# Kernel tuning notes

Hardware: AMD Instinct MI355X
Metric: run time of the kernel (lower is better)

Reference implementation:

```python
import jax, jax.numpy as jnp
import numpy as np

B, D, N, H, K = 8192, 1024, 4096, 8, 4
T, DECAY, STEPS = 100.0, 0.001, 3


def setup_inputs() -> dict:
    key = jax.random.key(0)
    ks = jax.random.split(key, 16)
    rn = lambda k, sh, s=0.02: jax.random.normal(k, sh, jnp.float32) * s
    return {
        'query': jax.random.normal(ks[0], (B, D), jnp.float32),
        'wm': jax.random.normal(ks[1], (B, D), jnp.float32),
        'keys': jax.random.normal(ks[2], (N, D), jnp.float32) * 0.1,
        'values': jax.random.normal(ks[3], (N, D), jnp.float32) * 0.1,
        'last_access': jax.random.uniform(ks[4], (N,), jnp.float32) * T,
        'importance': jnp.ones((N,), jnp.float32),
        'consolid': jnp.ones((N,), jnp.float32),
        'emo_tags': jax.random.uniform(ks[5], (N, 8), jnp.float32),
        'active': jnp.ones((N,), jnp.float32),
        'in_proj_w': rn(ks[6], (3 * D, D)), 'in_proj_b': jnp.zeros((3 * D,), jnp.float32),
        'out_w': rn(ks[7], (D, D)), 'out_b': jnp.zeros((D,), jnp.float32),
        'msg_w1': rn(ks[8], (D, 2 * D)), 'msg_b1': jnp.zeros((D,), jnp.float32),
        'msg_ln_g': jnp.ones((D,), jnp.float32), 'msg_ln_b': jnp.zeros((D,), jnp.float32),
        'msg_w2': rn(ks[9], (D, D)), 'msg_b2': jnp.zeros((D,), jnp.float32),
        'gru_wih': rn(ks[10], (3 * D, D)), 'gru_whh': rn(ks[11], (3 * D, D)),
        'gru_bih': jnp.zeros((3 * D,), jnp.float32), 'gru_bhh': jnp.zeros((3 * D,), jnp.float32),
        'rsn_w1': rn(ks[12], (D, D)), 'rsn_b1': jnp.zeros((D,), jnp.float32),
        'rsn_ln_g': jnp.ones((D,), jnp.float32), 'rsn_ln_b': jnp.zeros((D,), jnp.float32),
        'rsn_w2': rn(ks[13], (D, D)), 'rsn_b2': jnp.zeros((D,), jnp.float32),
        'top_k': K,
    }


def _ln(x, g, b):
    m = x.mean(-1, keepdims=True)
    v = ((x - m) ** 2).mean(-1, keepdims=True)
    return (x - m) / jnp.sqrt(v + 1e-5) * g + b


def reference(query, wm, keys, values, last_access, importance, consolid, emo_tags, active,
              in_proj_w, in_proj_b, out_w, out_b,
              msg_w1, msg_b1, msg_ln_g, msg_ln_b, msg_w2, msg_b2,
              gru_wih, gru_whh, gru_bih, gru_bhh,
              rsn_w1, rsn_b1, rsn_ln_g, rsn_ln_b, rsn_w2, rsn_b2, top_k):
    sg = jax.lax.stop_gradient
    # --- schema retrieve: cosine sim + forgetting-decay + boosts + topk softmax gather ---
    qn = query / jnp.maximum(jnp.linalg.norm(query, axis=-1, keepdims=True), 1e-8)
    kn = keys / jnp.maximum(jnp.linalg.norm(keys, axis=-1, keepdims=True), 1e-8)
    sims = qn @ kn.T  # [B, N]
    forget = sg(jnp.exp(-DECAY * (T - last_access)))
    boost = sg(emo_tags.sum(-1) * 0.1 + importance * 0.2 + jnp.log1p(consolid) * 0.1)
    scores = (sims * forget + boost) * sg(active)
    top_s, top_i = jax.lax.top_k(scores, top_k)  # [B, K]
    w = jax.nn.softmax(top_s, axis=-1)
    schema = jnp.einsum('bk,bkd->bd', w, values[top_i])  # [B, D]

    # --- GraphReasoner: 3 steps of 2-token MHA + msg_net + GRUCell ---
    dh = D // H
    scale = 1.0 / np.sqrt(dh).astype(np.float32)

    def mha(x):  # x [B, 2, D]
        qkv = x @ in_proj_w.T + in_proj_b
        q, k, v = jnp.split(qkv, 3, axis=-1)
        q = q.reshape(-1, 2, H, dh); k = k.reshape(-1, 2, H, dh); v = v.reshape(-1, 2, H, dh)
        a = jax.nn.softmax(jnp.einsum('bqhd,bkhd->bhqk', q, k) * scale, axis=-1)
        o = jnp.einsum('bhqk,bkhd->bqhd', a, v).reshape(-1, 2, D)
        return o @ out_w.T + out_b

    def gru(x, h):
        gi = x @ gru_wih.T + gru_bih
        gh = h @ gru_whh.T + gru_bhh
        ir, iz, inn = jnp.split(gi, 3, axis=-1)
        hr, hz, hn = jnp.split(gh, 3, axis=-1)
        r = jax.nn.sigmoid(ir + hr)
        z = jax.nn.sigmoid(iz + hz)
        n = jnp.tanh(inn + r * hn)
        return (1.0 - z) * n + z * h

    state = wm
    for _ in range(STEPS):
        ctx = jnp.stack([state, schema], axis=1)  # [B, 2, D]
        att = mha(ctx)
        combined = jnp.concatenate([att[:, 0], att[:, 1]], axis=-1)  # [B, 2D]
        msg = jax.nn.relu(_ln(combined @ msg_w1.T + msg_b1, msg_ln_g, msg_ln_b)) @ msg_w2.T + msg_b2
        state = gru(msg, state)
    out = jax.nn.relu(_ln(state @ rsn_w1.T + rsn_b1, rsn_ln_g, rsn_ln_b)) @ rsn_w2.T + rsn_b2
    return out
```

## Files before the change

### kernel.cpp

```cpp
#include <hip/hip_runtime.h>
#include <cstdint>
#include <cstddef>

typedef __attribute__((ext_vector_type(8))) short short8;
typedef __attribute__((ext_vector_type(4))) float f32x4;
typedef __attribute__((ext_vector_type(4))) unsigned short us4;

#define DEVINL static __device__ __forceinline__
#define AS1 __attribute__((address_space(1)))
#define AS3 __attribute__((address_space(3)))

DEVINL float bf2f(unsigned short u){
  union { unsigned uu; float f; } v; v.uu = ((unsigned)u) << 16; return v.f;
}
DEVINL unsigned short f2bf(float f){
  unsigned u = __float_as_uint(f);
  u += 0x7fffu + ((u >> 16) & 1u);
  return (unsigned short)(u >> 16);
}

DEVINL bool tk_better(float av, int ai, float bv, int bi){
  return (av > bv) || (av == bv && ai < bi);
}
DEVINL void tk_cmpex(float& va, int& ia, float& vb, int& ib){
  if (!tk_better(va, ia, vb, ib)){
    float tv = va; va = vb; vb = tv;
    int t = ia; ia = ib; ib = t;
  }
}
DEVINL void tk_sort4(float* v, int* id){
  tk_cmpex(v[0], id[0], v[1], id[1]);
  tk_cmpex(v[2], id[2], v[3], id[3]);
  tk_cmpex(v[0], id[0], v[2], id[2]);
  tk_cmpex(v[1], id[1], v[3], id[3]);
  tk_cmpex(v[1], id[1], v[2], id[2]);
}
DEVINL void tk_bmerge(float* v, int* id, const float* pv, const int* pi){
  #pragma unroll
  for (int i = 0; i < 4; ++i){
    bool ta = tk_better(v[i], id[i], pv[3 - i], pi[3 - i]);
    v[i]  = ta ? v[i]  : pv[3 - i];
    id[i] = ta ? id[i] : pi[3 - i];
  }
  tk_cmpex(v[0], id[0], v[2], id[2]);
  tk_cmpex(v[1], id[1], v[3], id[3]);
  tk_cmpex(v[0], id[0], v[1], id[1]);
  tk_cmpex(v[2], id[2], v[3], id[3]);
}

__global__ void k_diag(float* out, float v){ out[0] = v; }

__global__ __launch_bounds__(256) void k_cast_bf16(const float* __restrict__ x,
                                                   unsigned short* __restrict__ y, int n4){
  int stride = gridDim.x * blockDim.x;
  for (int i = blockIdx.x * blockDim.x + threadIdx.x; i < n4; i += stride){
    float4 v = ((const float4*)x)[i];
    us4 o; o[0] = f2bf(v.x); o[1] = f2bf(v.y); o[2] = f2bf(v.z); o[3] = f2bf(v.w);
    ((us4*)y)[i] = o;
  }
}

__global__ __launch_bounds__(256) void k_tcast(const float* __restrict__ in,
    unsigned short* __restrict__ outT, int R, int C){
  __shared__ float t[32][33];
  const int bc = blockIdx.x * 32, br = blockIdx.y * 32;
  const int lx = threadIdx.x & 31, ly = threadIdx.x >> 5;
  #pragma unroll
  for (int i = 0; i < 32; i += 8)
    t[ly + i][lx] = in[(size_t)(br + ly + i) * C + bc + lx];
  __syncthreads();
  #pragma unroll
  for (int i = 0; i < 32; i += 8)
    outT[(size_t)(bc + ly + i) * R + br + lx] = f2bf(t[lx][ly + i]);
}

__global__ __launch_bounds__(256) void k_bias_pre(const float* __restrict__ w1,
    const float* __restrict__ outb, const float* __restrict__ b1, float* __restrict__ bc){
  int wave = threadIdx.x >> 6, lane = threadIdx.x & 63;
  int j = blockIdx.x * 4 + wave;
  float s = 0.f;
  for (int m = lane; m < 2048; m += 64)
    s += w1[(size_t)j * 2048 + m] * outb[m & 1023];
  #pragma unroll
  for (int m = 32; m >= 1; m >>= 1) s += __shfl_xor(s, m);
  if (lane == 0) bc[j] = s + b1[j];
}

__global__ __launch_bounds__(256) void k_bias_gi(const float* __restrict__ wih,
    const float* __restrict__ b2, const float* __restrict__ bih, float* __restrict__ bc){
  int wave = threadIdx.x >> 6, lane = threadIdx.x & 63;
  int n = blockIdx.x * 4 + wave;
  float s = 0.f;
  for (int m = lane; m < 1024; m += 64)
    s += wih[(size_t)n * 1024 + m] * b2[m];
  #pragma unroll
  for (int m = 32; m >= 1; m >>= 1) s += __shfl_xor(s, m);
  if (lane == 0) bc[n] = s + bih[n];
}

__global__ __launch_bounds__(256) void k_prep_keys(const float* __restrict__ keys,
    const float* __restrict__ last_access, const float* __restrict__ importance,
    const float* __restrict__ consolid, const float* __restrict__ emo,
    const float* __restrict__ active, float* __restrict__ ascale, float* __restrict__ bbias){
  int wave = threadIdx.x >> 6, lane = threadIdx.x & 63;
  int n = blockIdx.x * 4 + wave;
  const float* kr = keys + (size_t)n * 1024;
  float s = 0.f;
  #pragma unroll
  for (int j = 0; j < 4; ++j){
    float4 v = ((const float4*)kr)[j * 64 + lane];
    s += v.x*v.x + v.y*v.y + v.z*v.z + v.w*v.w;
  }
  #pragma unroll
  for (int m = 32; m >= 1; m >>= 1) s += __shfl_xor(s, m);
  if (lane == 0){
    float norm = fmaxf(sqrtf(s), 1e-8f);
    float forget = expf(-0.001f * (100.0f - last_access[n]));
    float bo = 0.f;
    #pragma unroll
    for (int j = 0; j < 8; ++j) bo += emo[n * 8 + j];
    bo = bo * 0.1f + importance[n] * 0.2f + log1pf(consolid[n]) * 0.1f;
    float a = active[n];
    ascale[n] = forget * a / norm;
    bbias[n]  = bo * a;
  }
}

__global__ __launch_bounds__(256) void k_qnorm(const float* __restrict__ q, float* __restrict__ qinv){
  int wave = threadIdx.x >> 6, lane = threadIdx.x & 63;
  int b = blockIdx.x * 4 + wave;
  const float* qr = q + (size_t)b * 1024;
  float s = 0.f;
  #pragma unroll
  for (int j = 0; j < 4; ++j){
    float4 v = ((const float4*)qr)[j * 64 + lane];
    s += v.x*v.x + v.y*v.y + v.z*v.z + v.w*v.w;
  }
  #pragma unroll
  for (int m = 32; m >= 1; m >>= 1) s += __shfl_xor(s, m);
  if (lane == 0) qinv[b] = 1.0f / fmaxf(sqrtf(s), 1e-8f);
}

__global__ __launch_bounds__(256) void k_split(const float* __restrict__ X,
    const float* __restrict__ rscale, unsigned short* __restrict__ Hi,
    unsigned short* __restrict__ Lo){
  const int row = blockIdx.x;
  const float sc = rscale ? rscale[row] : 1.0f;
  const int d = threadIdx.x * 4;
  float4 v = *(const float4*)(X + (size_t)row * 1024 + d);
  float xs[4] = {v.x * sc, v.y * sc, v.z * sc, v.w * sc};
  us4 h, l;
  #pragma unroll
  for (int j = 0; j < 4; ++j){
    unsigned short hb = f2bf(xs[j]);
    h[j] = hb;
    l[j] = f2bf(xs[j] - bf2f(hb));
  }
  *(us4*)(Hi + (size_t)row * 1024 + d) = h;
  *(us4*)(Lo + (size_t)row * 1024 + d) = l;
}

__global__ __launch_bounds__(256) void k_scores_mfma(
    const unsigned short* __restrict__ Qhi, const unsigned short* __restrict__ Qlo,
    const unsigned short* __restrict__ Khi, const unsigned short* __restrict__ Klo,
    const float* __restrict__ ascale, const float* __restrict__ bbias,
    float* __restrict__ candV, int* __restrict__ candI){
  __shared__ __align__(16) unsigned short AsH[128 * 32];
  __shared__ __align__(16) unsigned short AsL[128 * 32];
  __shared__ __align__(16) unsigned short BsH[128 * 32];
  __shared__ __align__(16) unsigned short BsL[128 * 32];
  const int tid = threadIdx.x;
  const int wave = tid >> 6, lane = tid & 63;
  const int tM = blockIdx.x, tN = blockIdx.y;
  const int wm_ = wave >> 1, wn_ = wave & 1;
  f32x4 acc[4][4] = {};
  const unsigned short* AH = Qhi + (size_t)tM * 128 * 1024;
  const unsigned short* AL = Qlo + (size_t)tM * 128 * 1024;
  const unsigned short* BH = Khi + (size_t)tN * 128 * 1024;
  const unsigned short* BL = Klo + (size_t)tN * 128 * 1024;
  const int lrow = lane & 15, lk = (lane >> 4) * 8;
  for (int k0 = 0; k0 < 1024; k0 += 32){
    __syncthreads();
    #pragma unroll
    for (int j = 0; j < 2; ++j){
      int c = wave * 128 + j * 64 + lane;
      int row = c >> 2, cp = c & 3;
      size_t go = (size_t)row * 1024 + k0 + cp * 8;
      int lo_ = (wave * 2 + j) * 512;
      __builtin_amdgcn_global_load_lds((const AS1 void*)(AH + go), (AS3 void*)(AsH + lo_), 16, 0, 0);
      __builtin_amdgcn_global_load_lds((const AS1 void*)(AL + go), (AS3 void*)(AsL + lo_), 16, 0, 0);
      __builtin_amdgcn_global_load_lds((const AS1 void*)(BH + go), (AS3 void*)(BsH + lo_), 16, 0, 0);
      __builtin_amdgcn_global_load_lds((const AS1 void*)(BL + go), (AS3 void*)(BsL + lo_), 16, 0, 0);
    }
    __syncthreads();
    short8 ah[4], al[4], bh[4], bl[4];
    #pragma unroll
    for (int mi = 0; mi < 4; ++mi){
      int ro = (wm_ * 64 + mi * 16 + lrow) * 32 + lk;
      ah[mi] = *(const short8*)(AsH + ro);
      al[mi] = *(const short8*)(AsL + ro);
    }
    #pragma unroll
    for (int ni = 0; ni < 4; ++ni){
      int ro = (wn_ * 64 + ni * 16 + lrow) * 32 + lk;
      bh[ni] = *(const short8*)(BsH + ro);
      bl[ni] = *(const short8*)(BsL + ro);
    }
    #pragma unroll
    for (int mi = 0; mi < 4; ++mi)
      #pragma unroll
      for (int ni = 0; ni < 4; ++ni){
        acc[mi][ni] = __builtin_amdgcn_mfma_f32_16x16x32_bf16(ah[mi], bh[ni], acc[mi][ni], 0, 0, 0);
        acc[mi][ni] = __builtin_amdgcn_mfma_f32_16x16x32_bf16(ah[mi], bl[ni], acc[mi][ni], 0, 0, 0);
        acc[mi][ni] = __builtin_amdgcn_mfma_f32_16x16x32_bf16(al[mi], bh[ni], acc[mi][ni], 0, 0, 0);
      }
  }
  const int lc = lane & 15;
  float as_[4], bb_[4]; int cid[4];
  #pragma unroll
  for (int ni = 0; ni < 4; ++ni){
    cid[ni] = tN * 128 + wn_ * 64 + ni * 16 + lc;
    as_[ni] = ascale[cid[ni]];
    bb_[ni] = bbias[cid[ni]];
  }
  #pragma unroll
  for (int mi = 0; mi < 4; ++mi){
    #pragma unroll
    for (int r = 0; r < 4; ++r){
      float v[4]; int id[4];
      #pragma unroll
      for (int ni = 0; ni < 4; ++ni){
        v[ni]  = acc[mi][ni][r] * as_[ni] + bb_[ni];
        id[ni] = cid[ni];
      }
      tk_sort4(v, id);
      #pragma unroll
      for (int mask = 1; mask <= 8; mask <<= 1){
        float pv[4]; int pi_[4];
        #pragma unroll
        for (int j = 0; j < 4; ++j){
          pv[j]  = __shfl_xor(v[j], mask);
          pi_[j] = __shfl_xor(id[j], mask);
        }
        tk_bmerge(v, id, pv, pi_);
      }
      if (lc == 0){
        int row = tM * 128 + wm_ * 64 + mi * 16 + (lane >> 4) * 4 + r;
        size_t cb = (size_t)row * 256 + tN * 8 + wn_ * 4;
        #pragma unroll
        for (int j = 0; j < 4; ++j){ candV[cb + j] = v[j]; candI[cb + j] = id[j]; }
      }
    }
  }
}

__global__ __launch_bounds__(256) void k_topk_merge(const float* __restrict__ candV,
    const int* __restrict__ candI, const float* __restrict__ V,
    unsigned short* __restrict__ schema_bf){
  const int row = blockIdx.x, tid = threadIdx.x;
  const int wave = tid >> 6, lane = tid & 63;
  float v[4]; int id[4];
  v[0] = candV[(size_t)row * 256 + tid];
  id[0] = candI[(size_t)row * 256 + tid];
  #pragma unroll
  for (int j = 1; j < 4; ++j){ v[j] = -3.4e38f; id[j] = 0x7fffffff; }
  #pragma unroll
  for (int mask = 1; mask <= 32; mask <<= 1){
    float pv[4]; int pi_[4];
    #pragma unroll
    for (int j = 0; j < 4; ++j){
      pv[j]  = __shfl_xor(v[j], mask);
      pi_[j] = __shfl_xor(id[j], mask);
    }
    tk_bmerge(v, id, pv, pi_);
  }
  __shared__ float wv[4][4]; __shared__ int wi[4][4];
  if (lane == 0){
    #pragma unroll
    for (int j = 0; j < 4; ++j){ wv[wave][j] = v[j]; wi[wave][j] = id[j]; }
  }
  __syncthreads();
  __shared__ float w_sh[4]; __shared__ int i_sh[4];
  if (tid == 0){
    float fv[4]; int fi[4];
    #pragma unroll
    for (int j = 0; j < 4; ++j){ fv[j] = wv[0][j]; fi[j] = wi[0][j]; }
    #pragma unroll
    for (int w = 1; w < 4; ++w){
      float pv[4]; int pi_[4];
      #pragma unroll
      for (int j = 0; j < 4; ++j){ pv[j] = wv[w][j]; pi_[j] = wi[w][j]; }
      tk_bmerge(fv, fi, pv, pi_);
    }
    float m = fv[0];
    float e0 = expf(fv[0] - m), e1 = expf(fv[1] - m), e2 = expf(fv[2] - m), e3 = expf(fv[3] - m);
    float inv = 1.f / (e0 + e1 + e2 + e3);
    w_sh[0] = e0 * inv; w_sh[1] = e1 * inv; w_sh[2] = e2 * inv; w_sh[3] = e3 * inv;
    i_sh[0] = fi[0]; i_sh[1] = fi[1]; i_sh[2] = fi[2]; i_sh[3] = fi[3];
  }
  __syncthreads();
  float w0 = w_sh[0], w1 = w_sh[1], w2 = w_sh[2], w3 = w_sh[3];
  const float* v0 = V + (size_t)i_sh[0] * 1024;
  const float* v1 = V + (size_t)i_sh[1] * 1024;
  const float* v2 = V + (size_t)i_sh[2] * 1024;
  const float* v3 = V + (size_t)i_sh[3] * 1024;
  int d = tid * 4;
  float4 a = *(const float4*)(v0 + d);
  float4 b4 = *(const float4*)(v1 + d);
  float4 c = *(const float4*)(v2 + d);
  float4 e = *(const float4*)(v3 + d);
  us4 o;
  o[0] = f2bf(w0*a.x + w1*b4.x + w2*c.x + w3*e.x);
  o[1] = f2bf(w0*a.y + w1*b4.y + w2*c.y + w3*e.y);
  o[2] = f2bf(w0*a.z + w1*b4.z + w2*c.z + w3*e.z);
  o[3] = f2bf(w0*a.w + w1*b4.w + w2*c.w + w3*e.w);
  *(us4*)(schema_bf + (size_t)row * 1024 + d) = o;
}

__global__ __launch_bounds__(256) void k_initstate(const float* __restrict__ wm,
    float* __restrict__ st, unsigned short* __restrict__ stbf){
  size_t i = ((size_t)blockIdx.x * 256 + threadIdx.x) * 4;
  float4 v = *(const float4*)(wm + i);
  *(float4*)(st + i) = v;
  us4 o; o[0] = f2bf(v.x); o[1] = f2bf(v.y); o[2] = f2bf(v.z); o[3] = f2bf(v.w);
  *(us4*)(stbf + i) = o;
}

template<int OUT_BF16>
__global__ __launch_bounds__(256) void k_gemm(const unsigned short* __restrict__ A,
    const unsigned short* __restrict__ W, const float* __restrict__ bias,
    void* __restrict__ C, int M, int N, int K, int lda, int ldc){
  __shared__ __align__(16) unsigned short As[128 * 32];
  __shared__ __align__(16) unsigned short Ws[128 * 32];
  const int tid = threadIdx.x;
  const int wave = tid >> 6, lane = tid & 63;
  const int tM = blockIdx.x, tN = blockIdx.y;
  const int wm_ = wave >> 1, wn_ = wave & 1;
  f32x4 acc[4][4] = {};
  const unsigned short* Abase = A + (size_t)tM * 128 * lda;
  const unsigned short* Wbase = W + (size_t)tN * 128 * K;
  const int lrow = lane & 15, lk = (lane >> 4) * 8;
  for (int k0 = 0; k0 < K; k0 += 32){
    __syncthreads();
    #pragma unroll
    for (int j = 0; j < 2; ++j){
      int c = wave * 128 + j * 64 + lane;
      int row = c >> 2, cp = c & 3;
      const unsigned short* ga = Abase + (size_t)row * lda + k0 + cp * 8;
      const unsigned short* gw = Wbase + (size_t)row * K + k0 + cp * 8;
      __builtin_amdgcn_global_load_lds((const AS1 void*)ga, (AS3 void*)(As + (wave * 2 + j) * 512), 16, 0, 0);
      __builtin_amdgcn_global_load_lds((const AS1 void*)gw, (AS3 void*)(Ws + (wave * 2 + j) * 512), 16, 0, 0);
    }
    __syncthreads();
    short8 af[4], bfr[4];
    #pragma unroll
    for (int mi = 0; mi < 4; ++mi)
      af[mi] = *(const short8*)(As + (wm_ * 64 + mi * 16 + lrow) * 32 + lk);
    #pragma unroll
    for (int ni = 0; ni < 4; ++ni)
      bfr[ni] = *(const short8*)(Ws + (wn_ * 64 + ni * 16 + lrow) * 32 + lk);
    #pragma unroll
    for (int mi = 0; mi < 4; ++mi)
      #pragma unroll
      for (int ni = 0; ni < 4; ++ni)
        acc[mi][ni] = __builtin_amdgcn_mfma_f32_16x16x32_bf16(af[mi], bfr[ni], acc[mi][ni], 0, 0, 0);
  }
  const int lc = lane & 15, lr = (lane >> 4) * 4;
  #pragma unroll
  for (int ni = 0; ni < 4; ++ni){
    int col = tN * 128 + wn_ * 64 + ni * 16 + lc;
    float bb = bias ? bias[col] : 0.f;
    #pragma unroll
    for (int mi = 0; mi < 4; ++mi){
      int rowb = tM * 128 + wm_ * 64 + mi * 16 + lr;
      #pragma unroll
      for (int r = 0; r < 4; ++r){
        float vv = acc[mi][ni][r] + bb;
        size_t off = (size_t)(rowb + r) * ldc + col;
        if (OUT_BF16) ((unsigned short*)C)[off] = f2bf(vv);
        else ((float*)C)[off] = vv;
      }
    }
  }
}

template<int OUT_BF16>
__global__ __launch_bounds__(512, 2) void k_gemm8p(const unsigned short* __restrict__ A,
    const unsigned short* __restrict__ W, const float* __restrict__ bias,
    void* __restrict__ C, int M, int N, int K, int lda, int ldc){
  __shared__ __align__(16) unsigned short lds[65536];
  const int tid = threadIdx.x;
  const int wave = tid >> 6, lane = tid & 63;
  const int wqr = wave >> 2, wqc = wave & 3;
  const int lrow = lane & 15, lkk = lane >> 4;

  const int nwg = gridDim.x * gridDim.y;
  int lin = blockIdx.y * gridDim.x + blockIdx.x;
  int cpx = nwg >> 3;
  int swz = (lin & 7) * cpx + (lin >> 3);
  const int nM = M >> 8;
  const int tM = swz % nM, tN = swz / nM;

  const unsigned short* Abase = A + (size_t)tM * 256 * lda;
  const unsigned short* Wbase = W + (size_t)tN * 256 * K;

  f32x4 a00[4][2] = {}, a01[4][2] = {}, a11[4][2] = {}, a10[4][2] = {};
  short8 af[4][2], bf[2][2];
  const int ntiles = K >> 6;

  auto stage = [&](int op, int slot, int half, int tile){
    if (tile >= ntiles) return;
    const unsigned short* G = op ? Wbase : Abase;
    const int rs = op ? K : lda;
    const int k0 = tile * 64, hr = half * 128;
    const int base = op * 32768 + slot * 16384 + half * 8192;
    #pragma unroll
    for (int l = 0; l < 2; ++l){
      int p = l * 512 + tid;
      int row = p >> 3, c = (p & 7) ^ (row & 7);
      int dstc = l * 512 + wave * 64;
      __builtin_amdgcn_global_load_lds(
          (const AS1 void*)(G + (size_t)(hr + row) * rs + k0 + c * 8),
          (AS3 void*)(lds + base + dstc * 8), 16, 0, 0);
    }
  };
  auto ldA = [&](int slot, int half){
    const int base = slot * 16384 + half * 8192;
    #pragma unroll
    for (int mi = 0; mi < 4; ++mi)
      #pragma unroll
      for (int kk = 0; kk < 2; ++kk){
        int row = wqr * 64 + mi * 16 + lrow;
        int c = kk * 4 + lkk;
        af[mi][kk] = *(const short8*)(lds + base + (row * 8 + (c ^ (row & 7))) * 8);
      }
  };
  auto ldB = [&](int slot, int half){
    const int base = 32768 + slot * 16384 + half * 8192;
    #pragma unroll
    for (int ni = 0; ni < 2; ++ni)
      #pragma unroll
      for (int kk = 0; kk < 2; ++kk){
        int row = wqc * 32 + ni * 16 + lrow;
        int c = kk * 4 + lkk;
        bf[ni][kk] = *(const short8*)(lds + base + (row * 8 + (c ^ (row & 7))) * 8);
      }
  };
  auto mfma16 = [&](f32x4 (&acc)[4][2]){
    __builtin_amdgcn_s_setprio(1);
    #pragma unroll
    for (int mi = 0; mi < 4; ++mi)
      #pragma unroll
      for (int ni = 0; ni < 2; ++ni)
        #pragma unroll
        for (int kk = 0; kk < 2; ++kk)
          acc[mi][ni] = __builtin_amdgcn_mfma_f32_16x16x32_bf16(af[mi][kk], bf[ni][kk], acc[mi][ni], 0, 0, 0);
    __builtin_amdgcn_s_setprio(0);
  };
  auto SB = [&](){
    __builtin_amdgcn_sched_barrier(0);
    __builtin_amdgcn_s_barrier();
    __builtin_amdgcn_sched_barrier(0);
  };

  stage(0,0,0, 0); stage(1,0,0, 0); stage(1,0,1, 0); stage(0,0,1, 0);
  stage(0,1,0, 1); stage(1,1,1, 1);
  __builtin_amdgcn_sched_barrier(0);
  asm volatile("s_waitcnt vmcnt(4)" ::: "memory");
  __builtin_amdgcn_s_barrier();
  __builtin_amdgcn_sched_barrier(0);

  for (int j = 0; j < (ntiles >> 1); ++j){
    const int t0 = 2 * j;
    ldA(0,0); ldB(0,0); stage(0,1,1, t0+1);
    SB(); mfma16(a00); SB();
    ldB(0,1); stage(1,1,0, t0+1);
    SB(); mfma16(a01); SB();
    ldA(0,1); stage(0,0,0, t0+2);
    SB(); mfma16(a11); SB();
    ldB(0,0); stage(1,0,1, t0+2);
    SB(); mfma16(a10);
    __builtin_amdgcn_sched_barrier(0);
    if (t0 + 2 < ntiles) asm volatile("s_waitcnt vmcnt(4)" ::: "memory");
    else                 asm volatile("s_waitcnt vmcnt(0)" ::: "memory");
    __builtin_amdgcn_s_barrier();
    __builtin_amdgcn_sched_barrier(0);
    ldA(1,0); ldB(1,0); stage(0,0,1, t0+2);
    SB(); mfma16(a00); SB();
    ldB(1,1); stage(1,0,0, t0+2);
    SB(); mfma16(a01); SB();
    ldA(1,1); stage(0,1,0, t0+3);
    SB(); mfma16(a11); SB();
    ldB(1,0); stage(1,1,1, t0+3);
    SB(); mfma16(a10);
    __builtin_amdgcn_sched_barrier(0);
    asm volatile("s_waitcnt vmcnt(4)" ::: "memory");
    __builtin_amdgcn_s_barrier();
    __builtin_amdgcn_sched_barrier(0);
  }

  const int lc = lane & 15, lr = (lane >> 4) * 4;
  auto wout = [&](f32x4 (&acc)[4][2], int MH, int NH){
    #pragma unroll
    for (int ni = 0; ni < 2; ++ni){
      int col = tN * 256 + NH * 128 + wqc * 32 + ni * 16 + lc;
      float bb = bias ? bias[col] : 0.f;
      #pragma unroll
      for (int mi = 0; mi < 4; ++mi){
        int rowb = tM * 256 + MH * 128 + wqr * 64 + mi * 16 + lr;
        #pragma unroll
        for (int r = 0; r < 4; ++r){
          float vv = acc[mi][ni][r] + bb;
          size_t off = (size_t)(rowb + r) * ldc + col;
          if (OUT_BF16) ((unsigned short*)C)[off] = f2bf(vv);
          else ((float*)C)[off] = vv;
        }
      }
    }
  };
  wout(a00, 0, 0); wout(a01, 0, 1); wout(a11, 1, 1); wout(a10, 1, 0);
}

__global__ __launch_bounds__(256) void k_attn(unsigned short* qgh,
    const unsigned short* __restrict__ qkvM){
  const int b = blockIdx.x, tid = threadIdx.x;
  const int l = tid & 31;
  const int e = (tid >> 5) * 128 + l * 4;
  unsigned short* ps = qgh + (size_t)b * 6144;
  const unsigned short* pm = qkvM + (size_t)b * 3072;
  float q0[4], kk0[4], v0[4], q1[4], kk1[4], v1[4];
  us4 t;
  t = *(const us4*)(ps + e);        for (int j = 0; j < 4; ++j) q0[j]  = bf2f(t[j]);
  t = *(const us4*)(ps + 1024 + e); for (int j = 0; j < 4; ++j) kk0[j] = bf2f(t[j]);
  t = *(const us4*)(ps + 2048 + e); for (int j = 0; j < 4; ++j) v0[j]  = bf2f(t[j]);
  t = *(const us4*)(pm + e);        for (int j = 0; j < 4; ++j) q1[j]  = bf2f(t[j]);
  t = *(const us4*)(pm + 1024 + e); for (int j = 0; j < 4; ++j) kk1[j] = bf2f(t[j]);
  t = *(const us4*)(pm + 2048 + e); for (int j = 0; j < 4; ++j) v1[j]  = bf2f(t[j]);
  float s00 = 0.f, s01 = 0.f, s10 = 0.f, s11 = 0.f;
  #pragma unroll
  for (int j = 0; j < 4; ++j){
    s00 += q0[j] * kk0[j]; s01 += q0[j] * kk1[j];
    s10 += q1[j] * kk0[j]; s11 += q1[j] * kk1[j];
  }
  #pragma unroll
  for (int m = 16; m >= 1; m >>= 1){
    s00 += __shfl_xor(s00, m); s01 += __shfl_xor(s01, m);
    s10 += __shfl_xor(s10, m); s11 += __shfl_xor(s11, m);
  }
  const float sc = 0.08838834764831845f;
  s00 *= sc; s01 *= sc; s10 *= sc; s11 *= sc;
  float m0 = fmaxf(s00, s01), m1 = fmaxf(s10, s11);
  float e00 = expf(s00 - m0), e01 = expf(s01 - m0);
  float e10 = expf(s10 - m1), e11 = expf(s11 - m1);
  float i0 = 1.f / (e00 + e01), i1 = 1.f / (e10 + e11);
  float w00 = e00 * i0, w01 = e01 * i0, w10 = e10 * i1, w11 = e11 * i1;
  us4 o0, o1;
  #pragma unroll
  for (int j = 0; j < 4; ++j){
    o0[j] = f2bf(w00 * v0[j] + w01 * v1[j]);
    o1[j] = f2bf(w10 * v0[j] + w11 * v1[j]);
  }
  *(us4*)(ps + e)        = o0;
  *(us4*)(ps + 1024 + e) = o1;
}

template<int IN_BF16>
__global__ __launch_bounds__(256) void k_ln_relu(const void* X,
    const float* __restrict__ g, const float* __restrict__ bta, unsigned short* Y){
  const int row = blockIdx.x, tid = threadIdx.x;
  const int d = tid * 4;
  float e0, e1, e2, e3;
  if (IN_BF16){
    us4 t = *(const us4*)((const unsigned short*)X + (size_t)row * 1024 + d);
    e0 = bf2f(t[0]); e1 = bf2f(t[1]); e2 = bf2f(t[2]); e3 = bf2f(t[3]);
  } else {
    float4 v = *(const float4*)((const float*)X + (size_t)row * 1024 + d);
    e0 = v.x; e1 = v.y; e2 = v.z; e3 = v.w;
  }
  float s1 = e0 + e1 + e2 + e3;
  float s2 = e0*e0 + e1*e1 + e2*e2 + e3*e3;
  #pragma unroll
  for (int m = 32; m >= 1; m >>= 1){ s1 += __shfl_xor(s1, m); s2 += __shfl_xor(s2, m); }
  __shared__ float a1[4], a2[4];
  int wave = tid >> 6, lane = tid & 63;
  if (lane == 0){ a1[wave] = s1; a2[wave] = s2; }
  __syncthreads();
  s1 = a1[0] + a1[1] + a1[2] + a1[3];
  s2 = a2[0] + a2[1] + a2[2] + a2[3];
  float mean = s1 * (1.f / 1024.f);
  float var  = s2 * (1.f / 1024.f) - mean * mean;
  float rstd = rsqrtf(var + 1e-5f);
  float4 gg = *(const float4*)(g + d);
  float4 bb = *(const float4*)(bta + d);
  us4 o;
  o[0] = f2bf(fmaxf((e0 - mean) * rstd * gg.x + bb.x, 0.f));
  o[1] = f2bf(fmaxf((e1 - mean) * rstd * gg.y + bb.y, 0.f));
  o[2] = f2bf(fmaxf((e2 - mean) * rstd * gg.z + bb.z, 0.f));
  o[3] = f2bf(fmaxf((e3 - mean) * rstd * gg.w + bb.w, 0.f));
  *(us4*)(Y + (size_t)row * 1024 + d) = o;
}

__global__ __launch_bounds__(256) void k_gru(const unsigned short* __restrict__ qgh,
    const float* __restrict__ h, float* __restrict__ hn, unsigned short* __restrict__ hnbf){
  const int b = blockIdx.x;
  const int d = threadIdx.x * 4;
  const unsigned short* pi = qgh + (size_t)b * 6144;
  const unsigned short* ph = pi + 3072;
  us4 t;
  float ir[4], iz[4], in_[4], hr[4], hz[4], hnn[4];
  t = *(const us4*)(pi + d);        for (int j = 0; j < 4; ++j) ir[j]  = bf2f(t[j]);
  t = *(const us4*)(pi + 1024 + d); for (int j = 0; j < 4; ++j) iz[j]  = bf2f(t[j]);
  t = *(const us4*)(pi + 2048 + d); for (int j = 0; j < 4; ++j) in_[j] = bf2f(t[j]);
  t = *(const us4*)(ph + d);        for (int j = 0; j < 4; ++j) hr[j]  = bf2f(t[j]);
  t = *(const us4*)(ph + 1024 + d); for (int j = 0; j < 4; ++j) hz[j]  = bf2f(t[j]);
  t = *(const us4*)(ph + 2048 + d); for (int j = 0; j < 4; ++j) hnn[j] = bf2f(t[j]);
  float4 hv = *(const float4*)(h + (size_t)b * 1024 + d);
  float hvv[4] = {hv.x, hv.y, hv.z, hv.w};
  float ov[4]; us4 ob;
  #pragma unroll
  for (int j = 0; j < 4; ++j){
    float r = 1.f / (1.f + expf(-(ir[j] + hr[j])));
    float z = 1.f / (1.f + expf(-(iz[j] + hz[j])));
    float n = tanhf(in_[j] + r * hnn[j]);
    float o = (1.f - z) * n + z * hvv[j];
    ov[j] = o; ob[j] = f2bf(o);
  }
  float4 of; of.x = ov[0]; of.y = ov[1]; of.z = ov[2]; of.w = ov[3];
  *(float4*)(hn + (size_t)b * 1024 + d) = of;
  *(us4*)(hnbf + (size_t)b * 1024 + d) = ob;
}

extern "C" void kernel_launch(void* const* d_in, const int* in_sizes, int n_in,
                              void* d_out, int out_size, void* d_ws, size_t ws_size,
                              hipStream_t stream) {
  (void)in_sizes; (void)n_in; (void)out_size;
  const float* query       = (const float*)d_in[0];
  const float* wm          = (const float*)d_in[1];
  const float* keys        = (const float*)d_in[2];
  const float* values      = (const float*)d_in[3];
  const float* last_access = (const float*)d_in[4];
  const float* importance  = (const float*)d_in[5];
  const float* consolid    = (const float*)d_in[6];
  const float* emo         = (const float*)d_in[7];
  const float* active      = (const float*)d_in[8];
  const float* in_proj_w   = (const float*)d_in[9];
  const float* in_proj_b   = (const float*)d_in[10];
  const float* out_w       = (const float*)d_in[11];
  const float* out_b       = (const float*)d_in[12];
  const float* msg_w1      = (const float*)d_in[13];
  const float* msg_b1      = (const float*)d_in[14];
  const float* msg_ln_g    = (const float*)d_in[15];
  const float* msg_ln_b    = (const float*)d_in[16];
  const float* msg_w2      = (const float*)d_in[17];
  const float* msg_b2      = (const float*)d_in[18];
  const float* gru_wih     = (const float*)d_in[19];
  const float* gru_whh     = (const float*)d_in[20];
  const float* gru_bih     = (const float*)d_in[21];
  const float* gru_bhh     = (const float*)d_in[22];
  const float* rsn_w1      = (const float*)d_in[23];
  const float* rsn_b1      = (const float*)d_in[24];
  const float* rsn_ln_g    = (const float*)d_in[25];
  const float* rsn_ln_b    = (const float*)d_in[26];
  const float* rsn_w2      = (const float*)d_in[27];
  const float* rsn_b2      = (const float*)d_in[28];
  float* out = (float*)d_out;

  size_t off = 0;
  char* base = (char*)d_ws;
  auto carve = [&](size_t bytes) -> char* {
    char* p = base + off;
    off += (bytes + 255) & ~(size_t)255;
    return p;
  };
  float* ascale = (float*)carve(4096*4);
  float* bbias  = (float*)carve(4096*4);
  float* qinv   = (float*)carve(8192*4);
  float* bc_pre = (float*)carve(1024*4);
  float* bc_gi  = (float*)carve(3072*4);
  float* bc_ih  = (float*)carve(6144*4);
  unsigned short* wb_ihh  = (unsigned short*)carve((size_t)6144*1024*2);
  unsigned short* wb_rw1  = (unsigned short*)carve((size_t)1024*1024*2);
  unsigned short* wb_rw2  = (unsigned short*)carve((size_t)1024*1024*2);
  unsigned short* wb_Wab  = (unsigned short*)carve((size_t)1024*2048*2);
  unsigned short* wb_Wc   = (unsigned short*)carve((size_t)3072*1024*2);
  unsigned short* schema_bf = (unsigned short*)carve((size_t)8192*1024*2);
  float*          state_f   = (float*)carve((size_t)8192*1024*4);
  unsigned short* state_bf  = (unsigned short*)carve((size_t)8192*1024*2);
  unsigned short* qkvM      = (unsigned short*)carve((size_t)8192*3072*2);
  unsigned short* qgh       = (unsigned short*)carve((size_t)8192*6144*2);

  if (off > ws_size){
    k_diag<<<1, 1, 0, stream>>>(out, (float)(ws_size >> 20));
    return;
  }

  unsigned short* tmp_w1bf  = qgh;
  unsigned short* tmp_outwT = qgh + (size_t)1024*2048;
  unsigned short* tmp_w2T   = tmp_outwT + (size_t)1024*1024;
  unsigned short* tmp_wihbf = tmp_w2T + (size_t)1024*1024;

  unsigned short* Qhi = qkvM;
  unsigned short* Qlo = Qhi + (size_t)8192*1024;
  unsigned short* Khi = Qlo + (size_t)8192*1024;
  unsigned short* Klo = Khi + (size_t)4096*1024;
  float* candV = (float*)(qgh + (size_t)8192*3072);
  int*   candI = (int*)((char*)candV + (size_t)8192*256*4);

  unsigned short* preln_h1 = schema_bf;

  auto cast = [&](const float* src, unsigned short* dst, int n){
    k_cast_bf16<<<1024, 256, 0, stream>>>(src, dst, n / 4);
  };
  cast(in_proj_w, wb_ihh,                     3072*1024);
  cast(gru_whh,   wb_ihh + (size_t)3072*1024, 3072*1024);
  cast(rsn_w1,    wb_rw1,    1024*1024);
  cast(rsn_w2,    wb_rw2,    1024*1024);
  cast(msg_w1,    tmp_w1bf,  1024*2048);
  cast(gru_wih,   tmp_wihbf, 3072*1024);
  hipMemcpyAsync(bc_ih,        in_proj_b, 3072*4, hipMemcpyDeviceToDevice, stream);
  hipMemcpyAsync(bc_ih + 3072, gru_bhh,   3072*4, hipMemcpyDeviceToDevice, stream);
  k_tcast<<<dim3(32, 32), 256, 0, stream>>>(out_w,  tmp_outwT, 1024, 1024);
  k_tcast<<<dim3(32, 32), 256, 0, stream>>>(msg_w2, tmp_w2T,   1024, 1024);
  k_bias_pre<<<256, 256, 0, stream>>>(msg_w1, out_b, msg_b1, bc_pre);
  k_bias_gi<<<768, 256, 0, stream>>>(gru_wih, msg_b2, gru_bih, bc_gi);
  k_gemm<1><<<dim3(8, 8), 256, 0, stream>>>(tmp_w1bf,        tmp_outwT, nullptr, wb_Wab,        1024, 1024, 1024, 2048, 2048);
  k_gemm<1><<<dim3(8, 8), 256, 0, stream>>>(tmp_w1bf + 1024, tmp_outwT, nullptr, wb_Wab + 1024, 1024, 1024, 1024, 2048, 2048);
  k_gemm<1><<<dim3(24, 8), 256, 0, stream>>>(tmp_wihbf, tmp_w2T, nullptr, wb_Wc, 3072, 1024, 1024, 1024, 1024);

  k_qnorm<<<2048, 256, 0, stream>>>(query, qinv);
  k_prep_keys<<<1024, 256, 0, stream>>>(keys, last_access, importance, consolid, emo, active, ascale, bbias);
  k_split<<<8192, 256, 0, stream>>>(query, qinv, Qhi, Qlo);
  k_split<<<4096, 256, 0, stream>>>(keys, nullptr, Khi, Klo);
  k_scores_mfma<<<dim3(64, 32), 256, 0, stream>>>(Qhi, Qlo, Khi, Klo, ascale, bbias, candV, candI);
  k_topk_merge<<<8192, 256, 0, stream>>>(candV, candI, values, schema_bf);

  k_initstate<<<8192, 256, 0, stream>>>(wm, state_f, state_bf);
  k_gemm8p<1><<<dim3(32, 12), 512, 0, stream>>>(schema_bf, wb_ihh, bc_ih, qkvM, 8192, 3072, 1024, 1024, 3072);
  for (int s = 0; s < 3; ++s){
    k_gemm8p<1><<<dim3(32, 24), 512, 0, stream>>>(state_bf, wb_ihh, bc_ih, qgh, 8192, 6144, 1024, 1024, 6144);
    k_attn<<<8192, 256, 0, stream>>>(qgh, qkvM);
    k_gemm<1><<<dim3(64, 8), 256, 0, stream>>>(qgh, wb_Wab, bc_pre, preln_h1, 8192, 1024, 2048, 6144, 1024);
    k_ln_relu<1><<<8192, 256, 0, stream>>>(preln_h1, msg_ln_g, msg_ln_b, preln_h1);
    k_gemm8p<1><<<dim3(32, 12), 512, 0, stream>>>(preln_h1, wb_Wc, bc_gi, qgh, 8192, 3072, 1024, 1024, 6144);
    k_gru<<<8192, 256, 0, stream>>>(qgh, state_f, state_f, state_bf);
  }
  float* hpre = (float*)qgh;
  unsigned short* hh1 = qgh + (size_t)8192*3072;
  k_gemm<0><<<dim3(64, 8), 256, 0, stream>>>(state_bf, wb_rw1, rsn_b1, hpre, 8192, 1024, 1024, 1024, 1024);
  k_ln_relu<0><<<8192, 256, 0, stream>>>(hpre, rsn_ln_g, rsn_ln_b, hh1);
  k_gemm<0><<<dim3(64, 8), 256, 0, stream>>>(hh1, wb_rw2, rsn_b2, out, 8192, 1024, 1024, 1024, 1024);
}
```

Before: 1.502 ms.

## Rewrite retrieval scores GEMM as 256x256 pipelined kernel with concatenated split-bf16 K

The split-bf16 query and key operands are now laid out as single 3072-wide rows ([hi|lo|hi] against [hi|hi|lo]), so the three-term compensated product becomes one long-K GEMM. The scores kernel moves from a 128x128 tile with 256 threads and a sync-heavy loop to the 8-wave 256x256 ping-pong kernel. That kernel uses a swizzled LDS layout, double buffering, setprio and explicit waitcnt scheduling. The aim is higher MFMA utilisation and less global traffic per output. The cost is more scratch memory, duplicated hi writes, and a fixed grid of 512 workgroups.

```diff
diff --git a/kernel.cpp b/kernel.cpp
--- a/kernel.cpp
+++ b/kernel.cpp
@@ -141,9 +141,9 @@
   if (lane == 0) qinv[b] = 1.0f / fmaxf(sqrtf(s), 1e-8f);
 }
 
-__global__ __launch_bounds__(256) void k_split(const float* __restrict__ X,
-    const float* __restrict__ rscale, unsigned short* __restrict__ Hi,
-    unsigned short* __restrict__ Lo){
+__global__ __launch_bounds__(256) void k_split3(const float* __restrict__ X,
+    const float* __restrict__ rscale, unsigned short* __restrict__ D,
+    int offH1, int offH2, int offL){
   const int row = blockIdx.x;
   const float sc = rscale ? rscale[row] : 1.0f;
   const int d = threadIdx.x * 4;
@@ -156,102 +156,169 @@
     h[j] = hb;
     l[j] = f2bf(xs[j] - bf2f(hb));
   }
-  *(us4*)(Hi + (size_t)row * 1024 + d) = h;
-  *(us4*)(Lo + (size_t)row * 1024 + d) = l;
-}
-
-__global__ __launch_bounds__(256) void k_scores_mfma(
-    const unsigned short* __restrict__ Qhi, const unsigned short* __restrict__ Qlo,
-    const unsigned short* __restrict__ Khi, const unsigned short* __restrict__ Klo,
-    const float* __restrict__ ascale, const float* __restrict__ bbias,
-    float* __restrict__ candV, int* __restrict__ candI){
-  __shared__ __align__(16) unsigned short AsH[128 * 32];
-  __shared__ __align__(16) unsigned short AsL[128 * 32];
-  __shared__ __align__(16) unsigned short BsH[128 * 32];
-  __shared__ __align__(16) unsigned short BsL[128 * 32];
+  unsigned short* base = D + (size_t)row * 3072;
+  *(us4*)(base + offH1 + d) = h;
+  *(us4*)(base + offH2 + d) = h;
+  *(us4*)(base + offL  + d) = l;
+}
+
+__global__ __launch_bounds__(512, 2) void k_scores8p(const unsigned short* __restrict__ QX,
+    const unsigned short* __restrict__ KX, const float* __restrict__ ascale,
+    const float* __restrict__ bbias, float* __restrict__ candV, int* __restrict__ candI){
+  __shared__ __align__(16) unsigned short lds[65536];
   const int tid = threadIdx.x;
   const int wave = tid >> 6, lane = tid & 63;
-  const int tM = blockIdx.x, tN = blockIdx.y;
-  const int wm_ = wave >> 1, wn_ = wave & 1;
-  f32x4 acc[4][4] = {};
-  const unsigned short* AH = Qhi + (size_t)tM * 128 * 1024;
-  const unsigned short* AL = Qlo + (size_t)tM * 128 * 1024;
-  const unsigned short* BH = Khi + (size_t)tN * 128 * 1024;
-  const unsigned short* BL = Klo + (size_t)tN * 128 * 1024;
-  const int lrow = lane & 15, lk = (lane >> 4) * 8;
-  for (int k0 = 0; k0 < 1024; k0 += 32){
-    __syncthreads();
-    #pragma unroll
-    for (int j = 0; j < 2; ++j){
-      int c = wave * 128 + j * 64 + lane;
-      int row = c >> 2, cp = c & 3;
-      size_t go = (size_t)row * 1024 + k0 + cp * 8;
-      int lo_ = (wave * 2 + j) * 512;
-      __builtin_amdgcn_global_load_lds((const AS1 void*)(AH + go), (AS3 void*)(AsH + lo_), 16, 0, 0);
-      __builtin_amdgcn_global_load_lds((const AS1 void*)(AL + go), (AS3 void*)(AsL + lo_), 16, 0, 0);
-      __builtin_amdgcn_global_load_lds((const AS1 void*)(BH + go), (AS3 void*)(BsH + lo_), 16, 0, 0);
-      __builtin_amdgcn_global_load_lds((const AS1 void*)(BL + go), (AS3 void*)(BsL + lo_), 16, 0, 0);
+  const int wqr = wave >> 2, wqc = wave & 3;
+  const int lrow = lane & 15, lkk = lane >> 4;
+  const int K = 3072;
+
+  const int nwg = gridDim.x * gridDim.y;
+  int lin = blockIdx.y * gridDim.x + blockIdx.x;
+  int cpx = nwg >> 3;
+  int swz = (lin & 7) * cpx + (lin >> 3);
+  const int nM = 32;
+  const int tM = swz % nM, tN = swz / nM;
+
+  const unsigned short* Abase = QX + (size_t)tM * 256 * K;
+  const unsigned short* Wbase = KX + (size_t)tN * 256 * K;
+
+  f32x4 a00[4][2] = {}, a01[4][2] = {}, a11[4][2] = {}, a10[4][2] = {};
+  short8 af[4][2], bf[2][2];
+  const int ntiles = K >> 6;
+
+  auto stage = [&](int op, int slot, int half, int tile){
+    if (tile >= ntiles) return;
+    const unsigned short* G = op ? Wbase : Abase;
+    const int k0 = tile * 64, hr = half * 128;
+    const int base = op * 32768 + slot * 16384 + half * 8192;
+    #pragma unroll
+    for (int l = 0; l < 2; ++l){
+      int p = l * 512 + tid;
+      int row = p >> 3, c = (p & 7) ^ (row & 7);
+      int dstc = l * 512 + wave * 64;
+      __builtin_amdgcn_global_load_lds(
+          (const AS1 void*)(G + (size_t)(hr + row) * K + k0 + c * 8),
+          (AS3 void*)(lds + base + dstc * 8), 16, 0, 0);
     }
-    __syncthreads();
-    short8 ah[4], al[4], bh[4], bl[4];
+  };
+  auto ldA = [&](int slot, int half){
+    const int base = slot * 16384 + half * 8192;
+    #pragma unroll
+    for (int mi = 0; mi < 4; ++mi)
+      #pragma unroll
+      for (int kk = 0; kk < 2; ++kk){
+        int row = wqr * 64 + mi * 16 + lrow;
+        int c = kk * 4 + lkk;
+        af[mi][kk] = *(const short8*)(lds + base + (row * 8 + (c ^ (row & 7))) * 8);
+      }
+  };
+  auto ldB = [&](int slot, int half){
+    const int base = 32768 + slot * 16384 + half * 8192;
+    #pragma unroll
+    for (int ni = 0; ni < 2; ++ni)
+      #pragma unroll
+      for (int kk = 0; kk < 2; ++kk){
+        int row = wqc * 32 + ni * 16 + lrow;
+        int c = kk * 4 + lkk;
+        bf[ni][kk] = *(const short8*)(lds + base + (row * 8 + (c ^ (row & 7))) * 8);
+      }
+  };
+  auto mfma16 = [&](f32x4 (&acc)[4][2]){
+    __builtin_amdgcn_s_setprio(1);
+    #pragma unroll
+    for (int mi = 0; mi < 4; ++mi)
+      #pragma unroll
+      for (int ni = 0; ni < 2; ++ni)
+        #pragma unroll
+        for (int kk = 0; kk < 2; ++kk)
+          acc[mi][ni] = __builtin_amdgcn_mfma_f32_16x16x32_bf16(af[mi][kk], bf[ni][kk], acc[mi][ni], 0, 0, 0);
+    __builtin_amdgcn_s_setprio(0);
+  };
+  auto SB = [&](){
+    __builtin_amdgcn_sched_barrier(0);
+    __builtin_amdgcn_s_barrier();
+    __builtin_amdgcn_sched_barrier(0);
+  };
+
+  stage(0,0,0, 0); stage(1,0,0, 0); stage(1,0,1, 0); stage(0,0,1, 0);
+  stage(0,1,0, 1); stage(1,1,1, 1);
+  __builtin_amdgcn_sched_barrier(0);
+  asm volatile("s_waitcnt vmcnt(4)" ::: "memory");
+  __builtin_amdgcn_s_barrier();
+  __builtin_amdgcn_sched_barrier(0);
+
+  for (int j = 0; j < (ntiles >> 1); ++j){
+    const int t0 = 2 * j;
+    ldA(0,0); ldB(0,0); stage(0,1,1, t0+1);
+    SB(); mfma16(a00); SB();
+    ldB(0,1); stage(1,1,0, t0+1);
+    SB(); mfma16(a01); SB();
+    ldA(0,1); stage(0,0,0, t0+2);
+    SB(); mfma16(a11); SB();
+    ldB(0,0); stage(1,0,1, t0+2);
+    SB(); mfma16(a10);
+    __builtin_amdgcn_sched_barrier(0);
+    if (t0 + 2 < ntiles) asm volatile("s_waitcnt vmcnt(4)" ::: "memory");
+    else                 asm volatile("s_waitcnt vmcnt(0)" ::: "memory");
+    __builtin_amdgcn_s_barrier();
+    __builtin_amdgcn_sched_barrier(0);
+    ldA(1,0); ldB(1,0); stage(0,0,1, t0+2);
+    SB(); mfma16(a00); SB();
+    ldB(1,1); stage(1,0,0, t0+2);
+    SB(); mfma16(a01); SB();
+    ldA(1,1); stage(0,1,0, t0+3);
+    SB(); mfma16(a11); SB();
+    ldB(1,0); stage(1,1,1, t0+3);
+    SB(); mfma16(a10);
+    __builtin_amdgcn_sched_barrier(0);
+    asm volatile("s_waitcnt vmcnt(4)" ::: "memory");
+    __builtin_amdgcn_s_barrier();
+    __builtin_amdgcn_sched_barrier(0);
+  }
+
+  const int lc = lane & 15, lgrp = lane >> 4;
+  float as_[2][2], bb_[2][2]; int cid[2][2];
+  #pragma unroll
+  for (int NH = 0; NH < 2; ++NH)
+    #pragma unroll
+    for (int ni = 0; ni < 2; ++ni){
+      int col = tN * 256 + NH * 128 + wqc * 32 + ni * 16 + lc;
+      cid[NH][ni] = col;
+      as_[NH][ni] = ascale[col];
+      bb_[NH][ni] = bbias[col];
+    }
+  auto epi = [&](f32x4 (&n0)[4][2], f32x4 (&n1)[4][2], int MH){
     #pragma unroll
     for (int mi = 0; mi < 4; ++mi){
-      int ro = (wm_ * 64 + mi * 16 + lrow) * 32 + lk;
-      ah[mi] = *(const short8*)(AsH + ro);
-      al[mi] = *(const short8*)(AsL + ro);
-    }
-    #pragma unroll
-    for (int ni = 0; ni < 4; ++ni){
-      int ro = (wn_ * 64 + ni * 16 + lrow) * 32 + lk;
-      bh[ni] = *(const short8*)(BsH + ro);
-      bl[ni] = *(const short8*)(BsL + ro);
-    }
-    #pragma unroll
-    for (int mi = 0; mi < 4; ++mi)
-      #pragma unroll
-      for (int ni = 0; ni < 4; ++ni){
-        acc[mi][ni] = __builtin_amdgcn_mfma_f32_16x16x32_bf16(ah[mi], bh[ni], acc[mi][ni], 0, 0, 0);
-        acc[mi][ni] = __builtin_amdgcn_mfma_f32_16x16x32_bf16(ah[mi], bl[ni], acc[mi][ni], 0, 0, 0);
-        acc[mi][ni] = __builtin_amdgcn_mfma_f32_16x16x32_bf16(al[mi], bh[ni], acc[mi][ni], 0, 0, 0);
-      }
-  }
-  const int lc = lane & 15;
-  float as_[4], bb_[4]; int cid[4];
-  #pragma unroll
-  for (int ni = 0; ni < 4; ++ni){
-    cid[ni] = tN * 128 + wn_ * 64 + ni * 16 + lc;
-    as_[ni] = ascale[cid[ni]];
-    bb_[ni] = bbias[cid[ni]];
-  }
-  #pragma unroll
-  for (int mi = 0; mi < 4; ++mi){
-    #pragma unroll
-    for (int r = 0; r < 4; ++r){
-      float v[4]; int id[4];
-      #pragma unroll
-      for (int ni = 0; ni < 4; ++ni){
-        v[ni]  = acc[mi][ni][r] * as_[ni] + bb_[ni];
-        id[ni] = cid[ni];
-      }
-      tk_sort4(v, id);
-      #pragma unroll
-      for (int mask = 1; mask <= 8; mask <<= 1){
-        float pv[4]; int pi_[4];
+      #pragma unroll
+      for (int r = 0; r < 4; ++r){
+        float v[4]; int id[4];
+        v[0] = n0[mi][0][r] * as_[0][0] + bb_[0][0]; id[0] = cid[0][0];
+        v[1] = n0[mi][1][r] * as_[0][1] + bb_[0][1]; id[1] = cid[0][1];
+        v[2] = n1[mi][0][r] * as_[1][0] + bb_[1][0]; id[2] = cid[1][0];
+        v[3] = n1[mi][1][r] * as_[1][1] + bb_[1][1]; id[3] = cid[1][1];
+        tk_sort4(v, id);
         #pragma unroll
-        for (int j = 0; j < 4; ++j){
-          pv[j]  = __shfl_xor(v[j], mask);
-          pi_[j] = __shfl_xor(id[j], mask);
+        for (int mask = 1; mask <= 8; mask <<= 1){
+          float pv[4]; int pi_[4];
+          #pragma unroll
+          for (int jj = 0; jj < 4; ++jj){
+            pv[jj]  = __shfl_xor(v[jj], mask);
+            pi_[jj] = __shfl_xor(id[jj], mask);
+          }
+          tk_bmerge(v, id, pv, pi_);
         }
-        tk_bmerge(v, id, pv, pi_);
-      }
-      if (lc == 0){
-        int row = tM * 128 + wm_ * 64 + mi * 16 + (lane >> 4) * 4 + r;
-        size_t cb = (size_t)row * 256 + tN * 8 + wn_ * 4;
-        #pragma unroll
-        for (int j = 0; j < 4; ++j){ candV[cb + j] = v[j]; candI[cb + j] = id[j]; }
+        if (lc == 0){
+          int row = tM * 256 + MH * 128 + wqr * 64 + mi * 16 + lgrp * 4 + r;
+          size_t cb = (size_t)row * 256 + tN * 16 + wqc * 4;
+          #pragma unroll
+          for (int jj = 0; jj < 4; ++jj){ candV[cb + jj] = v[jj]; candI[cb + jj] = id[jj]; }
+        }
       }
     }
-  }
+  };
+  epi(a00, a01, 0);
+  epi(a10, a11, 1);
 }
 
 __global__ __launch_bounds__(256) void k_topk_merge(const float* __restrict__ candV,
@@ -694,15 +761,13 @@
     return;
   }
 
-  unsigned short* tmp_w1bf  = qgh;
-  unsigned short* tmp_outwT = qgh + (size_t)1024*2048;
+  unsigned short* tmp_w1bf  = qgh + (size_t)8192*3072;
+  unsigned short* tmp_outwT = tmp_w1bf + (size_t)1024*2048;
   unsigned short* tmp_w2T   = tmp_outwT + (size_t)1024*1024;
   unsigned short* tmp_wihbf = tmp_w2T + (size_t)1024*1024;
 
-  unsigned short* Qhi = qkvM;
-  unsigned short* Qlo = Qhi + (size_t)8192*1024;
-  unsigned short* Khi = Qlo + (size_t)8192*1024;
-  unsigned short* Klo = Khi + (size_t)4096*1024;
+  unsigned short* QX = qkvM;
+  unsigned short* KX = qgh;
   float* candV = (float*)(qgh + (size_t)8192*3072);
   int*   candI = (int*)((char*)candV + (size_t)8192*256*4);
 
@@ -729,9 +794,9 @@
 
   k_qnorm<<<2048, 256, 0, stream>>>(query, qinv);
   k_prep_keys<<<1024, 256, 0, stream>>>(keys, last_access, importance, consolid, emo, active, ascale, bbias);
-  k_split<<<8192, 256, 0, stream>>>(query, qinv, Qhi, Qlo);
-  k_split<<<4096, 256, 0, stream>>>(keys, nullptr, Khi, Klo);
-  k_scores_mfma<<<dim3(64, 32), 256, 0, stream>>>(Qhi, Qlo, Khi, Klo, ascale, bbias, candV, candI);
+  k_split3<<<8192, 256, 0, stream>>>(query, qinv, QX, 0, 2048, 1024);
+  k_split3<<<4096, 256, 0, stream>>>(keys, nullptr, KX, 0, 1024, 2048);
+  k_scores8p<<<dim3(32, 16), 512, 0, stream>>>(QX, KX, ascale, bbias, candV, candI);
   k_topk_merge<<<8192, 256, 0, stream>>>(candV, candI, values, schema_bf);
 
   k_initstate<<<8192, 256, 0, stream>>>(wm, state_f, state_bf);
```

New measurement: 1.506 ms. No clear change (+0.3%).
